# Kernel optimization log

Measured on AMD Instinct MI355X. Metric: run time of the kernel, lower is better.

Reference implementation:

```python
import jax, jax.numpy as jnp
import numpy as np

D_X = 16
D_L = 8
T_LEN = 131072
BIN_THRES = 0.1


def setup_inputs() -> dict:
    key = jax.random.key(0)
    ks = jax.random.split(key, 24)
    n = lambda k, shp, sc=0.1: jax.random.normal(k, shp, jnp.float32) * sc
    inp = {
        "latent_mean": jax.random.normal(ks[0], (2, T_LEN, D_L), jnp.float32),
        "latent_logvar": jax.random.normal(ks[1], (2, T_LEN, D_L), jnp.float32),
        "T": jax.random.uniform(ks[2], (T_LEN, 1), jnp.float32),
        # curr_adj_encoder: MLP(1 -> d_L -> d_L -> d_L*d_X), lrelu
        "cw0": n(ks[3], (1, D_L)), "cb0": n(ks[4], (D_L,)),
        "cw1": n(ks[5], (D_L, D_L)), "cb1": n(ks[6], (D_L,)),
        "cw2": n(ks[7], (D_L, D_L * D_X)), "cb2": n(ks[8], (D_L * D_X,)),
        # pre_adj_encoder
        "pw0": n(ks[9], (1, D_L)), "pb0": n(ks[10], (D_L,)),
        "pw1": n(ks[11], (D_L, D_L)), "pb1": n(ks[12], (D_L,)),
        "pw2": n(ks[13], (D_L, D_L * D_X)), "pb2": n(ks[14], (D_L * D_X,)),
        # latent_mean_out: FeatureExtractor(d_L,128,relu) + Linear(128,d_L)
        "fmw1": n(ks[15], (D_L, 128)), "fmb1": jnp.zeros((128,), jnp.float32),
        "fmw2": n(ks[16], (128, D_L)), "fmb2": jnp.zeros((D_L,), jnp.float32),
        # latent_logvar_out
        "fvw1": n(ks[17], (D_L, 128)), "fvb1": jnp.zeros((128,), jnp.float32),
        "fvw2": n(ks[18], (128, D_L)), "fvb2": jnp.zeros((D_L,), jnp.float32),
        # L2M per-node MLPs, batched over d_X: 4*d_L -> 64 -> 64 -> 1
        "lw0": n(ks[19], (D_X, 4 * D_L, 64)), "lb0": jnp.zeros((D_X, 64), jnp.float32),
        "lw1": n(ks[20], (D_X, 64, 64)), "lb1": jnp.zeros((D_X, 64), jnp.float32),
        "lw2": n(ks[21], (D_X, 64, 1)), "lb2": jnp.zeros((D_X, 1), jnp.float32),
    }
    return inp


def _forward(latent_mean, latent_logvar, T,
             cw0, cb0, cw1, cb1, cw2, cb2,
             pw0, pb0, pw1, pb1, pw2, pb2,
             fmw1, fmb1, fmw2, fmb2,
             fvw1, fvb1, fvw2, fvb2,
             lw0, lb0, lw1, lb1, lw2, lb2):
    lrelu = jax.nn.leaky_relu

    def mlp(x, w0, b0, w1, b1, w2, b2):
        h = lrelu(x @ w0 + b0)
        h = lrelu(h @ w1 + b1)
        return h @ w2 + b2

    Ct = mlp(T, cw0, cb0, cw1, cb1, cw2, cb2).reshape(-1, D_X, D_L)
    Ct_1 = mlp(T, pw0, pb0, pw1, pb1, pw2, pb2).reshape(-1, D_X, D_L)
    # Only Ct is binarized in the original forward (Ct_1 stays continuous).
    Ct = jnp.where(Ct < BIN_THRES, 0.0, 1.0).astype(Ct.dtype)

    zeros = jnp.zeros_like(latent_mean[:, :1, :])
    lm_prev = jnp.concatenate([zeros, latent_mean[:, :-1, :]], axis=1)
    lv_prev = jnp.concatenate([zeros, latent_logvar[:, :-1, :]], axis=1)

    def head(x, w1, b1, w2, b2):
        return jax.nn.relu(x @ w1 + b1) @ w2 + b2

    lm_pred = head(latent_mean, fmw1, fmb1, fmw2, fmb2)
    lv_pred = head(latent_logvar, fvw1, fvb1, fvw2, fvb2)

    def decode(lm, lv, C):
        # C: [T, d_X, d_L]; lm/lv: [2, T, d_L]
        def gather(x):
            g = jnp.einsum('ijk,lik->lijk', C, x)          # [2, T, d_X, d_L]
            g = jnp.transpose(g, (1, 2, 3, 0))              # [T, d_X, d_L, 2]
            return g.reshape(x.shape[1], D_X, 2 * D_L)
        h = jnp.concatenate([gather(lm), gather(lv)], axis=-1)  # [T, d_X, 4*d_L]
        h = jax.nn.relu(jnp.einsum('tnf,nfo->tno', h, lw0) + lb0)
        h = jnp.einsum('tnf,nfo->tno', h, lw1) + lb1             # last decoder layer: no relu
        h = jnp.einsum('tnf,nfo->tno', h, lw2) + lb2             # [T, d_X, 1]
        return jax.nn.relu(h[..., 0])                             # [T, d_X]

    recon = decode(latent_mean, latent_logvar, Ct)
    pred = decode(lm_prev, lv_prev, Ct_1)
    return recon, pred, lm_pred, lv_pred, Ct, Ct_1


def reference(latent_mean, latent_logvar, T,
              cw0, cb0, cw1, cb1, cw2, cb2,
              pw0, pb0, pw1, pb1, pw2, pb2,
              fmw1, fmb1, fmw2, fmb2,
              fvw1, fvb1, fvw2, fvb2,
              lw0, lb0, lw1, lb1, lw2, lb2):
    return _forward(latent_mean, latent_logvar, T,
                    cw0, cb0, cw1, cb1, cw2, cb2,
                    pw0, pb0, pw1, pb1, pw2, pb2,
                    fmw1, fmb1, fmw2, fmb2,
                    fvw1, fvb1, fvw2, fvb2,
                    lw0, lb0, lw1, lb1, lw2, lb2)
```

## Files before the change

### kernel.cpp

```cpp
#include <hip/hip_runtime.h>
#include <math.h>

#define TL 131072

static constexpr size_t OFF_RECON = 0;
static constexpr size_t OFF_PRED  = (size_t)TL * 16;
static constexpr size_t OFF_LMP   = (size_t)TL * 32;
static constexpr size_t OFF_LVP   = (size_t)TL * 48;
static constexpr size_t OFF_CT    = (size_t)TL * 64;
static constexpr size_t OFF_CT1   = (size_t)TL * 192;

typedef _Float16 h2 __attribute__((ext_vector_type(2)));
typedef _Float16 h8 __attribute__((ext_vector_type(8)));
typedef float f32x4 __attribute__((ext_vector_type(4)));

struct Params {
  const float* lm;  const float* lv;  const float* Tin;
  const float* cw0; const float* cb0; const float* cw1; const float* cb1; const float* cw2; const float* cb2;
  const float* pw0; const float* pb0; const float* pw1; const float* pb1; const float* pw2; const float* pb2;
  const float* fmw1; const float* fmb1; const float* fmw2; const float* fmb2;
  const float* fvw1; const float* fvb1; const float* fvw2; const float* fvb2;
  const float* lw0; const float* lb0; const float* lw1; const float* lb1; const float* lw2; const float* lb2;
  const float* w12src;
  float* out;
};

__device__ __forceinline__ const float4* rc4(const float* p) { return reinterpret_cast<const float4*>(p); }
__device__ __forceinline__ float4*       rw4(float* p)       { return reinterpret_cast<float4*>(p); }

__device__ __forceinline__ void load8(const float* __restrict__ src, float* dst) {
  float4 a = rc4(src)[0], b = rc4(src)[1];
  dst[0]=a.x; dst[1]=a.y; dst[2]=a.z; dst[3]=a.w;
  dst[4]=b.x; dst[5]=b.y; dst[6]=b.z; dst[7]=b.w;
}
__device__ __forceinline__ void store8(float* __restrict__ dst, const float* v) {
  rw4(dst)[0] = make_float4(v[0],v[1],v[2],v[3]);
  rw4(dst)[1] = make_float4(v[4],v[5],v[6],v[7]);
}
__device__ __forceinline__ void store16(float* __restrict__ dst, const float* v) {
  rw4(dst)[0] = make_float4(v[0],v[1],v[2],v[3]);
  rw4(dst)[1] = make_float4(v[4],v[5],v[6],v[7]);
  rw4(dst)[2] = make_float4(v[8],v[9],v[10],v[11]);
  rw4(dst)[3] = make_float4(v[12],v[13],v[14],v[15]);
}

union PU { h2 h; uint32_t u; };
union U4 { uint32_t u[4]; h2 h[4]; h8 v; uint4 q; };

__device__ __forceinline__ h2 pack2(float a, float b) {
  h2 r; r[0] = (_Float16)a; r[1] = (_Float16)b; return r;
}

__global__ __launch_bounds__(256) void tld_prep(const float* __restrict__ lw1,
                                                const float* __restrict__ lw2,
                                                const float* __restrict__ lb1,
                                                const float* __restrict__ lb2,
                                                float* __restrict__ ws) {
  const int tid = threadIdx.x;
  #pragma unroll 1
  for (int i = tid; i < 1024; i += 256) {
    int n = i >> 6, h = i & 63;
    float s = 0.f;
    #pragma unroll 8
    for (int o = 0; o < 64; ++o)
      s = fmaf(lw1[n * 4096 + h * 64 + o], lw2[n * 64 + o], s);
    ws[i] = s;
  }
  if (tid < 16) {
    float b = lb2[tid];
    #pragma unroll 8
    for (int o = 0; o < 64; ++o)
      b = fmaf(lb1[tid * 64 + o], lw2[tid * 64 + o], b);
    ws[1024 + tid] = b;
  }
}

__global__ __launch_bounds__(256, 2) void tld_fused(Params p) {
  __shared__ __align__(16) float     s_w12[1024];
  __shared__ __align__(16) float     s_b12[16];
  __shared__ __align__(16) float     s_lb0[1024];
  __shared__ __align__(16) float     s_ew2t[128 * 8];
  __shared__ __align__(16) float     s_eb2b[128];
  __shared__ __align__(16) float     s_hw1t[2][1024];
  __shared__ __align__(16) float     s_hw2[2][1024];
  __shared__ __align__(16) float     s_hb1[2][128];
  __shared__ __align__(16) float     s_hb2[2][8];
  __shared__ __align__(16) _Float16  s_W[2][64 * 40];
  __shared__ __align__(16) uint32_t  s_dl[129 * 20];
  __shared__ __align__(16) float     s_e1[128 * 12];
  __shared__ __align__(16) unsigned long long s_msk[128 * 3];
  __shared__ __align__(16) float     s_res[4][16 * 68];

  const int tid = threadIdx.x;
  const int B   = blockIdx.x * 128;

  rw4(s_lb0)[tid]    = rc4(p.lb0)[tid];
  rw4(s_hw2[0])[tid] = rc4(p.fmw2)[tid];
  rw4(s_hw2[1])[tid] = rc4(p.fvw2)[tid];
  if (tid < 32)       { rw4(s_hb1[0])[tid] = rc4(p.fmb1)[tid]; }
  else if (tid < 64)  { rw4(s_hb1[1])[tid - 32] = rc4(p.fvb1)[tid - 32]; }
  else if (tid < 96)  { rw4(s_eb2b)[tid - 64] = rc4(p.pb2)[tid - 64]; }
  else if (tid < 100) { int q = tid - 96; rw4(s_hb2[q >> 1])[q & 1] = rc4((q >> 1) ? p.fvb2 : p.fmb2)[q & 1]; }
  #pragma unroll 1
  for (int i = tid; i < 2048; i += 256) {
    int r = i >> 10, ii = i & 1023, o = ii >> 3, f = ii & 7;
    s_hw1t[r][ii] = (r ? p.fvw1 : p.fmw1)[f * 128 + o];
  }
  if (tid < 128) {
    #pragma unroll
    for (int i = 0; i < 8; ++i) s_ew2t[tid * 8 + i] = p.pw2[i * 128 + tid];
  }
  if (p.w12src) {
    rw4(s_w12)[tid] = rc4(p.w12src)[tid];
    if (tid < 4) rw4(s_b12)[tid] = rc4(p.w12src + 1024)[tid];
  } else {
    #pragma unroll 1
    for (int i = tid; i < 1024; i += 256) {
      int n = i >> 6, h = i & 63;
      float s = 0.f;
      for (int o = 0; o < 64; ++o)
        s = fmaf(p.lw1[n * 4096 + h * 64 + o], p.lw2[n * 64 + o], s);
      s_w12[i] = s;
    }
    if (tid < 16) {
      float b = p.lb2[tid];
      for (int o = 0; o < 64; ++o)
        b = fmaf(p.lb1[tid * 64 + o], p.lw2[tid * 64 + o], b);
      s_b12[tid] = b;
    }
  }
  const int wk  = tid & 31;
  const int wj0 = (tid >> 5) * 8;
  {
    const float4* g = rc4(p.lw0);
    float4 wa = g[wk * 16 + (tid >> 5) * 2];
    float4 wb = g[wk * 16 + (tid >> 5) * 2 + 1];
    _Float16* dW = s_W[0];
    dW[(wj0 + 0) * 40 + wk] = (_Float16)wa.x;
    dW[(wj0 + 1) * 40 + wk] = (_Float16)wa.y;
    dW[(wj0 + 2) * 40 + wk] = (_Float16)wa.z;
    dW[(wj0 + 3) * 40 + wk] = (_Float16)wa.w;
    dW[(wj0 + 4) * 40 + wk] = (_Float16)wb.x;
    dW[(wj0 + 5) * 40 + wk] = (_Float16)wb.y;
    dW[(wj0 + 6) * 40 + wk] = (_Float16)wb.z;
    dW[(wj0 + 7) * 40 + wk] = (_Float16)wb.w;
  }
  __syncthreads();

  const int u    = tid & 127;
  const int t    = B + u;
  const int role = __builtin_amdgcn_readfirstlane((int)(tid >> 7));
  const float Tt = p.Tin[t];

  unsigned long long cmlo = 0ull, cmhi = 0ull;
  float e1f[8];

  if (role == 0) {
    double e0d[8], e1d[8];
    const double Td = (double)Tt;
    #pragma unroll
    for (int j = 0; j < 8; ++j) {
      double v = Td * (double)p.cw0[j] + (double)p.cb0[j];
      e0d[j] = v < 0.0 ? 0.01 * v : v;
    }
    #pragma unroll
    for (int j = 0; j < 8; ++j) {
      double v = (double)p.cb1[j];
      #pragma unroll
      for (int i = 0; i < 8; ++i) v = fma(e0d[i], (double)p.cw1[i * 8 + j], v);
      e1d[j] = v < 0.0 ? 0.01 * v : v;
    }
    #pragma unroll 1
    for (int n2 = 0; n2 < 8; ++n2) {
      float cb[16];
      #pragma unroll
      for (int kk = 0; kk < 16; ++kk) {
        const int nk = n2 * 16 + kk;
        double s = (double)p.cb2[nk];
        #pragma unroll
        for (int i = 0; i < 8; ++i)
          s = fma(e1d[i], (double)p.cw2[i * 128 + nk], s);
        const int b = (s < 0.1) ? 0 : 1;
        cb[kk] = (float)b;
        if (nk < 64) cmlo |= (unsigned long long)b << nk;
        else         cmhi |= (unsigned long long)b << (nk - 64);
      }
      store16(p.out + OFF_CT + (size_t)t * 128 + n2 * 16, cb);
    }
    s_msk[u * 3]     = cmlo;
    s_msk[u * 3 + 1] = cmhi;
  } else {
    float e0[8];
    #pragma unroll
    for (int j = 0; j < 8; ++j) {
      float v = fmaf(Tt, p.pw0[j], p.pb0[j]);
      e0[j] = v < 0.f ? 0.01f * v : v;
    }
    #pragma unroll
    for (int j = 0; j < 8; ++j) {
      float v = p.pb1[j];
      #pragma unroll
      for (int i = 0; i < 8; ++i) v = fmaf(e0[i], p.pw1[i * 8 + j], v);
      e1f[j] = v < 0.f ? 0.01f * v : v;
    }
    {
      float4* d = (float4*)&s_e1[u * 12];
      d[0] = make_float4(e1f[0], e1f[1], e1f[2], e1f[3]);
      d[1] = make_float4(e1f[4], e1f[5], e1f[6], e1f[7]);
    }
    #pragma unroll 1
    for (int n2 = 0; n2 < 8; ++n2) {
      float cb[16];
      #pragma unroll
      for (int kk = 0; kk < 16; ++kk) {
        const int nk = n2 * 16 + kk;
        const float4* w = (const float4*)&s_ew2t[nk * 8];
        float4 x0 = w[0], x1 = w[1];
        float s = s_eb2b[nk];
        s = fmaf(e1f[0], x0.x, s); s = fmaf(e1f[1], x0.y, s);
        s = fmaf(e1f[2], x0.z, s); s = fmaf(e1f[3], x0.w, s);
        s = fmaf(e1f[4], x1.x, s); s = fmaf(e1f[5], x1.y, s);
        s = fmaf(e1f[6], x1.z, s); s = fmaf(e1f[7], x1.w, s);
        cb[kk] = s;
      }
      store16(p.out + OFF_CT1 + (size_t)t * 128 + n2 * 16, cb);
    }
  }

  float dl[4][8];
  if (role == 0) {
    load8(p.lm + (size_t)t * 8, dl[0]);
    load8(p.lm + (size_t)TL * 8 + (size_t)t * 8, dl[1]);
    load8(p.lv + (size_t)t * 8, dl[2]);
    load8(p.lv + (size_t)TL * 8 + (size_t)t * 8, dl[3]);
  } else {
    if (t > 0) {
      load8(p.lm + (size_t)(t - 1) * 8, dl[0]);
      load8(p.lm + (size_t)TL * 8 + (size_t)(t - 1) * 8, dl[1]);
      load8(p.lv + (size_t)(t - 1) * 8, dl[2]);
      load8(p.lv + (size_t)TL * 8 + (size_t)(t - 1) * 8, dl[3]);
    } else {
      #pragma unroll
      for (int r = 0; r < 4; ++r)
        #pragma unroll
        for (int j = 0; j < 8; ++j) dl[r][j] = 0.f;
    }
  }
  {
    const int slot = (role == 0) ? (u + 1) : (u == 0 ? 0 : -1);
    if (slot >= 0) {
      uint32_t dw[16];
      #pragma unroll
      for (int k = 0; k < 8; ++k) {
        PU a; a.h = pack2(dl[0][k], dl[1][k]); dw[k]     = a.u;
        PU b; b.h = pack2(dl[2][k], dl[3][k]); dw[8 + k] = b.u;
      }
      uint4* dst = (uint4*)&s_dl[slot * 20];
      dst[0] = make_uint4(dw[0], dw[1], dw[2], dw[3]);
      dst[1] = make_uint4(dw[4], dw[5], dw[6], dw[7]);
      dst[2] = make_uint4(dw[8], dw[9], dw[10], dw[11]);
      dst[3] = make_uint4(dw[12], dw[13], dw[14], dw[15]);
    }
  }

  {
    float hx[2][8];
    if (role == 0) {
      #pragma unroll
      for (int j = 0; j < 8; ++j) { hx[0][j] = dl[0][j]; hx[1][j] = dl[1][j]; }
    } else {
      load8(p.lv + (size_t)t * 8, hx[0]);
      load8(p.lv + (size_t)TL * 8 + (size_t)t * 8, hx[1]);
    }
    float acc8[2][8];
    #pragma unroll
    for (int l = 0; l < 2; ++l)
      #pragma unroll
      for (int j = 0; j < 8; ++j) acc8[l][j] = s_hb2[role][j];
    const float* w1t = s_hw1t[role];
    const float* w2r = s_hw2[role];
    const float* b1  = s_hb1[role];
    #pragma unroll 1
    for (int o = 0; o < 128; ++o) {
      float4 u0 = rc4(w1t)[o * 2], u1 = rc4(w1t)[o * 2 + 1];
      const float wf[8] = {u0.x,u0.y,u0.z,u0.w,u1.x,u1.y,u1.z,u1.w};
      const float bo = b1[o];
      float a0 = bo, a1 = bo;
      #pragma unroll
      for (int f = 0; f < 8; ++f) {
        a0 = fmaf(hx[0][f], wf[f], a0);
        a1 = fmaf(hx[1][f], wf[f], a1);
      }
      a0 = fmaxf(a0, 0.f); a1 = fmaxf(a1, 0.f);
      float4 v0 = rc4(w2r)[o * 2], v1 = rc4(w2r)[o * 2 + 1];
      const float w2f[8] = {v0.x,v0.y,v0.z,v0.w,v1.x,v1.y,v1.z,v1.w};
      #pragma unroll
      for (int j = 0; j < 8; ++j) {
        acc8[0][j] = fmaf(a0, w2f[j], acc8[0][j]);
        acc8[1][j] = fmaf(a1, w2f[j], acc8[1][j]);
      }
    }
    const size_t hbase = role ? OFF_LVP : OFF_LMP;
    store8(p.out + hbase + (size_t)t * 8, acc8[0]);
    store8(p.out + hbase + (size_t)TL * 8 + (size_t)t * 8, acc8[1]);
  }

  __syncthreads();

  const int w     = tid >> 6;
  const int lane  = tid & 63;
  const int drole = __builtin_amdgcn_readfirstlane(w >> 1);
  const int tl0   = (w & 1) * 64;
  const int l15   = lane & 15;
  const int g     = lane >> 4;
  const int kb    = (g & 1) * 4;
  float* res = s_res[w];

  #pragma unroll 1
  for (int n = 0; n < 16; ++n) {
    float4 wa, wb;
    if (n < 15) {
      const float4* gsrc = rc4(p.lw0 + (size_t)(n + 1) * 2048);
      wa = gsrc[wk * 16 + (tid >> 5) * 2];
      wb = gsrc[wk * 16 + (tid >> 5) * 2 + 1];
    }
    float cwv[4][8];
    if (drole == 1) {
      #pragma unroll
      for (int q = 0; q < 4; ++q) {
        const float4* ww = (const float4*)&s_ew2t[(n * 8 + kb + q) * 8];
        float4 x0 = ww[0], x1 = ww[1];
        cwv[q][0]=x0.x; cwv[q][1]=x0.y; cwv[q][2]=x0.z; cwv[q][3]=x0.w;
        cwv[q][4]=x1.x; cwv[q][5]=x1.y; cwv[q][6]=x1.z; cwv[q][7]=x1.w;
      }
    }
    const _Float16* Wcur = s_W[n & 1];
    h8 Bf[4];
    float bias[4], w12v[4];
    #pragma unroll
    for (int ji = 0; ji < 4; ++ji) {
      Bf[ji]   = *(const h8*)&Wcur[(ji * 16 + l15) * 40 + g * 8];
      bias[ji] = s_lb0[n * 64 + ji * 16 + l15];
      w12v[ji] = s_w12[n * 64 + ji * 16 + l15];
    }
    h8 Af[4];
    #pragma unroll
    for (int ti = 0; ti < 4; ++ti) {
      const int tloc = tl0 + ti * 16 + l15;
      const int slot = tloc + 1 - drole;
      U4 dv; dv.q = *(const uint4*)&s_dl[slot * 20 + g * 4];
      U4 xf;
      if (drole == 0) {
        const unsigned long long m = s_msk[tloc * 3 + (n >> 3)];
        const unsigned byte = (unsigned)(m >> ((n & 7) * 8)) & 0xffu;
        #pragma unroll
        for (int q = 0; q < 4; ++q)
          xf.u[q] = ((byte >> (kb + q)) & 1u) ? dv.u[q] : 0u;
      } else {
        const float4* e = (const float4*)&s_e1[tloc * 12];
        float4 e0 = e[0], e1v = e[1];
        const float ef[8] = {e0.x,e0.y,e0.z,e0.w,e1v.x,e1v.y,e1v.z,e1v.w};
        #pragma unroll
        for (int q = 0; q < 4; ++q) {
          float c = s_eb2b[n * 8 + kb + q];
          #pragma unroll
          for (int i = 0; i < 8; ++i) c = fmaf(ef[i], cwv[q][i], c);
          xf.h[q] = pack2(c, c) * dv.h[q];
        }
      }
      Af[ti] = xf.v;
    }
    const float b12n = s_b12[n];
    #pragma unroll
    for (int ti = 0; ti < 4; ++ti) {
      f32x4 d0, d1, d2, d3;
      d0[0]=bias[0]; d0[1]=bias[0]; d0[2]=bias[0]; d0[3]=bias[0];
      d1[0]=bias[1]; d1[1]=bias[1]; d1[2]=bias[1]; d1[3]=bias[1];
      d2[0]=bias[2]; d2[1]=bias[2]; d2[2]=bias[2]; d2[3]=bias[2];
      d3[0]=bias[3]; d3[1]=bias[3]; d3[2]=bias[3]; d3[3]=bias[3];
      d0 = __builtin_amdgcn_mfma_f32_16x16x32_f16(Af[ti], Bf[0], d0, 0, 0, 0);
      d1 = __builtin_amdgcn_mfma_f32_16x16x32_f16(Af[ti], Bf[1], d1, 0, 0, 0);
      d2 = __builtin_amdgcn_mfma_f32_16x16x32_f16(Af[ti], Bf[2], d2, 0, 0, 0);
      d3 = __builtin_amdgcn_mfma_f32_16x16x32_f16(Af[ti], Bf[3], d3, 0, 0, 0);
      float pr[4];
      #pragma unroll
      for (int reg = 0; reg < 4; ++reg) {
        float s = fmaxf(d0[reg], 0.f) * w12v[0];
        s = fmaf(fmaxf(d1[reg], 0.f), w12v[1], s);
        s = fmaf(fmaxf(d2[reg], 0.f), w12v[2], s);
        s = fmaf(fmaxf(d3[reg], 0.f), w12v[3], s);
        pr[reg] = s;
      }
      #pragma unroll
      for (int m = 1; m < 16; m <<= 1) {
        #pragma unroll
        for (int reg = 0; reg < 4; ++reg)
          pr[reg] += __shfl_xor(pr[reg], m, 64);
      }
      #pragma unroll
      for (int reg = 0; reg < 4; ++reg)
        pr[reg] = fmaxf(b12n + pr[reg], 0.f);
      if (l15 == 0) {
        float4* d = (float4*)&res[n * 68 + ti * 16 + g * 4];
        d[0] = make_float4(pr[0], pr[1], pr[2], pr[3]);
      }
    }
    if (n < 15) {
      _Float16* dW = s_W[(n + 1) & 1];
      dW[(wj0 + 0) * 40 + wk] = (_Float16)wa.x;
      dW[(wj0 + 1) * 40 + wk] = (_Float16)wa.y;
      dW[(wj0 + 2) * 40 + wk] = (_Float16)wa.z;
      dW[(wj0 + 3) * 40 + wk] = (_Float16)wa.w;
      dW[(wj0 + 4) * 40 + wk] = (_Float16)wb.x;
      dW[(wj0 + 5) * 40 + wk] = (_Float16)wb.y;
      dW[(wj0 + 6) * 40 + wk] = (_Float16)wb.z;
      dW[(wj0 + 7) * 40 + wk] = (_Float16)wb.w;
    }
    __syncthreads();
  }

  {
    float o16[16];
    #pragma unroll
    for (int n = 0; n < 16; ++n) o16[n] = res[n * 68 + lane];
    const size_t r_off = drole ? OFF_PRED : OFF_RECON;
    store16(p.out + r_off + (size_t)(B + tl0 + lane) * 16, o16);
  }
}

extern "C" void kernel_launch(void* const* d_in, const int* in_sizes, int n_in,
                              void* d_out, int out_size, void* d_ws, size_t ws_size,
                              hipStream_t stream) {
  Params p;
  p.lm   = (const float*)d_in[0];
  p.lv   = (const float*)d_in[1];
  p.Tin  = (const float*)d_in[2];
  p.cw0  = (const float*)d_in[3];  p.cb0 = (const float*)d_in[4];
  p.cw1  = (const float*)d_in[5];  p.cb1 = (const float*)d_in[6];
  p.cw2  = (const float*)d_in[7];  p.cb2 = (const float*)d_in[8];
  p.pw0  = (const float*)d_in[9];  p.pb0 = (const float*)d_in[10];
  p.pw1  = (const float*)d_in[11]; p.pb1 = (const float*)d_in[12];
  p.pw2  = (const float*)d_in[13]; p.pb2 = (const float*)d_in[14];
  p.fmw1 = (const float*)d_in[15]; p.fmb1 = (const float*)d_in[16];
  p.fmw2 = (const float*)d_in[17]; p.fmb2 = (const float*)d_in[18];
  p.fvw1 = (const float*)d_in[19]; p.fvb1 = (const float*)d_in[20];
  p.fvw2 = (const float*)d_in[21]; p.fvb2 = (const float*)d_in[22];
  p.lw0  = (const float*)d_in[23]; p.lb0 = (const float*)d_in[24];
  p.lw1  = (const float*)d_in[25]; p.lb1 = (const float*)d_in[26];
  p.lw2  = (const float*)d_in[27]; p.lb2 = (const float*)d_in[28];
  p.out  = (float*)d_out;

  const bool use_ws = ws_size >= 1040 * sizeof(float);
  if (use_ws) {
    tld_prep<<<dim3(1), dim3(256), 0, stream>>>(p.lw1, p.lw2, p.lb1, p.lb2, (float*)d_ws);
    p.w12src = (const float*)d_ws;
  } else {
    p.w12src = nullptr;
  }
  tld_fused<<<dim3(TL / 128), dim3(256), 0, stream>>>(p);
}
```

Measured before the change: 466.8 us.

## Swap MFMA operand roles, read C from global, alias LDS to raise occupancy

```diff
diff --git a/kernel.cpp b/kernel.cpp
--- a/kernel.cpp
+++ b/kernel.cpp
@@ -44,7 +44,6 @@
   rw4(dst)[3] = make_float4(v[12],v[13],v[14],v[15]);
 }
 
-union PU { h2 h; uint32_t u; };
 union U4 { uint32_t u[4]; h2 h[4]; h8 v; uint4 q; };
 
 __device__ __forceinline__ h2 pack2(float a, float b) {
@@ -75,36 +74,35 @@
   }
 }
 
-__global__ __launch_bounds__(256, 2) void tld_fused(Params p) {
-  __shared__ __align__(16) float     s_w12[1024];
-  __shared__ __align__(16) float     s_b12[16];
-  __shared__ __align__(16) float     s_lb0[1024];
-  __shared__ __align__(16) float     s_ew2t[128 * 8];
-  __shared__ __align__(16) float     s_eb2b[128];
-  __shared__ __align__(16) float     s_hw1t[2][1024];
-  __shared__ __align__(16) float     s_hw2[2][1024];
-  __shared__ __align__(16) float     s_hb1[2][128];
-  __shared__ __align__(16) float     s_hb2[2][8];
-  __shared__ __align__(16) _Float16  s_W[2][64 * 40];
-  __shared__ __align__(16) uint32_t  s_dl[129 * 20];
-  __shared__ __align__(16) float     s_e1[128 * 12];
-  __shared__ __align__(16) unsigned long long s_msk[128 * 3];
-  __shared__ __align__(16) float     s_res[4][16 * 68];
+__global__ __launch_bounds__(256, 4) void tld_fused(Params p) {
+  __shared__ __align__(16) _Float16 s_W[2][64 * 40];
+  __shared__ __align__(16) float    s_w12[1024];
+  __shared__ __align__(16) float    s_b12[16];
+  __shared__ __align__(16) float    s_lb0[1024];
+  __shared__ __align__(16) char     s_pool[22080];
+
+  float* s_hw1t = (float*)s_pool;
+  float* s_hw2  = (float*)(s_pool + 8192);
+  float* s_hb1  = (float*)(s_pool + 16384);
+  float* s_hb2  = (float*)(s_pool + 17408);
+  float* s_ew2t = (float*)(s_pool + 17472);
+  float* s_eb2b = (float*)(s_pool + 21568);
+  _Float16* s_resh = (_Float16*)s_pool;
 
   const int tid = threadIdx.x;
   const int B   = blockIdx.x * 128;
 
-  rw4(s_lb0)[tid]    = rc4(p.lb0)[tid];
-  rw4(s_hw2[0])[tid] = rc4(p.fmw2)[tid];
-  rw4(s_hw2[1])[tid] = rc4(p.fvw2)[tid];
-  if (tid < 32)       { rw4(s_hb1[0])[tid] = rc4(p.fmb1)[tid]; }
-  else if (tid < 64)  { rw4(s_hb1[1])[tid - 32] = rc4(p.fvb1)[tid - 32]; }
+  rw4(s_lb0)[tid]          = rc4(p.lb0)[tid];
+  rw4(s_hw2)[tid]          = rc4(p.fmw2)[tid];
+  rw4(s_hw2 + 1024)[tid]   = rc4(p.fvw2)[tid];
+  if (tid < 32)       { rw4(s_hb1)[tid] = rc4(p.fmb1)[tid]; }
+  else if (tid < 64)  { rw4(s_hb1 + 128)[tid - 32] = rc4(p.fvb1)[tid - 32]; }
   else if (tid < 96)  { rw4(s_eb2b)[tid - 64] = rc4(p.pb2)[tid - 64]; }
-  else if (tid < 100) { int q = tid - 96; rw4(s_hb2[q >> 1])[q & 1] = rc4((q >> 1) ? p.fvb2 : p.fmb2)[q & 1]; }
+  else if (tid < 100) { int q = tid - 96; rw4(s_hb2 + (q >> 1) * 8)[q & 1] = rc4((q >> 1) ? p.fvb2 : p.fmb2)[q & 1]; }
   #pragma unroll 1
   for (int i = tid; i < 2048; i += 256) {
     int r = i >> 10, ii = i & 1023, o = ii >> 3, f = ii & 7;
-    s_hw1t[r][ii] = (r ? p.fvw1 : p.fmw1)[f * 128 + o];
+    s_hw1t[r * 1024 + ii] = (r ? p.fvw1 : p.fmw1)[f * 128 + o];
   }
   if (tid < 128) {
     #pragma unroll
@@ -152,9 +150,6 @@
   const int role = __builtin_amdgcn_readfirstlane((int)(tid >> 7));
   const float Tt = p.Tin[t];
 
-  unsigned long long cmlo = 0ull, cmhi = 0ull;
-  float e1f[8];
-
   if (role == 0) {
     double e0d[8], e1d[8];
     const double Td = (double)Tt;
@@ -180,17 +175,12 @@
         #pragma unroll
         for (int i = 0; i < 8; ++i)
           s = fma(e1d[i], (double)p.cw2[i * 128 + nk], s);
-        const int b = (s < 0.1) ? 0 : 1;
-        cb[kk] = (float)b;
-        if (nk < 64) cmlo |= (unsigned long long)b << nk;
-        else         cmhi |= (unsigned long long)b << (nk - 64);
+        cb[kk] = (s < 0.1) ? 0.f : 1.f;
       }
       store16(p.out + OFF_CT + (size_t)t * 128 + n2 * 16, cb);
     }
-    s_msk[u * 3]     = cmlo;
-    s_msk[u * 3 + 1] = cmhi;
   } else {
-    float e0[8];
+    float e0[8], e1f[8];
     #pragma unroll
     for (int j = 0; j < 8; ++j) {
       float v = fmaf(Tt, p.pw0[j], p.pb0[j]);
@@ -202,11 +192,6 @@
       #pragma unroll
       for (int i = 0; i < 8; ++i) v = fmaf(e0[i], p.pw1[i * 8 + j], v);
       e1f[j] = v < 0.f ? 0.01f * v : v;
-    }
-    {
-      float4* d = (float4*)&s_e1[u * 12];
-      d[0] = make_float4(e1f[0], e1f[1], e1f[2], e1f[3]);
-      d[1] = make_float4(e1f[4], e1f[5], e1f[6], e1f[7]);
     }
     #pragma unroll 1
     for (int n2 = 0; n2 < 8; ++n2) {
@@ -227,59 +212,24 @@
     }
   }
 
-  float dl[4][8];
-  if (role == 0) {
-    load8(p.lm + (size_t)t * 8, dl[0]);
-    load8(p.lm + (size_t)TL * 8 + (size_t)t * 8, dl[1]);
-    load8(p.lv + (size_t)t * 8, dl[2]);
-    load8(p.lv + (size_t)TL * 8 + (size_t)t * 8, dl[3]);
-  } else {
-    if (t > 0) {
-      load8(p.lm + (size_t)(t - 1) * 8, dl[0]);
-      load8(p.lm + (size_t)TL * 8 + (size_t)(t - 1) * 8, dl[1]);
-      load8(p.lv + (size_t)(t - 1) * 8, dl[2]);
-      load8(p.lv + (size_t)TL * 8 + (size_t)(t - 1) * 8, dl[3]);
-    } else {
-      #pragma unroll
-      for (int r = 0; r < 4; ++r)
-        #pragma unroll
-        for (int j = 0; j < 8; ++j) dl[r][j] = 0.f;
-    }
-  }
-  {
-    const int slot = (role == 0) ? (u + 1) : (u == 0 ? 0 : -1);
-    if (slot >= 0) {
-      uint32_t dw[16];
-      #pragma unroll
-      for (int k = 0; k < 8; ++k) {
-        PU a; a.h = pack2(dl[0][k], dl[1][k]); dw[k]     = a.u;
-        PU b; b.h = pack2(dl[2][k], dl[3][k]); dw[8 + k] = b.u;
-      }
-      uint4* dst = (uint4*)&s_dl[slot * 20];
-      dst[0] = make_uint4(dw[0], dw[1], dw[2], dw[3]);
-      dst[1] = make_uint4(dw[4], dw[5], dw[6], dw[7]);
-      dst[2] = make_uint4(dw[8], dw[9], dw[10], dw[11]);
-      dst[3] = make_uint4(dw[12], dw[13], dw[14], dw[15]);
-    }
-  }
-
   {
     float hx[2][8];
     if (role == 0) {
-      #pragma unroll
-      for (int j = 0; j < 8; ++j) { hx[0][j] = dl[0][j]; hx[1][j] = dl[1][j]; }
+      load8(p.lm + (size_t)t * 8, hx[0]);
+      load8(p.lm + (size_t)TL * 8 + (size_t)t * 8, hx[1]);
     } else {
       load8(p.lv + (size_t)t * 8, hx[0]);
       load8(p.lv + (size_t)TL * 8 + (size_t)t * 8, hx[1]);
     }
+    const float* w1t  = s_hw1t + role * 1024;
+    const float* w2r  = s_hw2  + role * 1024;
+    const float* b1   = s_hb1  + role * 128;
+    const float* hb2r = s_hb2  + role * 8;
     float acc8[2][8];
     #pragma unroll
     for (int l = 0; l < 2; ++l)
       #pragma unroll
-      for (int j = 0; j < 8; ++j) acc8[l][j] = s_hb2[role][j];
-    const float* w1t = s_hw1t[role];
-    const float* w2r = s_hw2[role];
-    const float* b1  = s_hb1[role];
+      for (int j = 0; j < 8; ++j) acc8[l][j] = hb2r[j];
     #pragma unroll 1
     for (int o = 0; o < 128; ++o) {
       float4 u0 = rc4(w1t)[o * 2], u1 = rc4(w1t)[o * 2 + 1];
@@ -314,7 +264,27 @@
   const int l15   = lane & 15;
   const int g     = lane >> 4;
   const int kb    = (g & 1) * 4;
-  float* res = s_res[w];
+  const float* xbase = (g < 2) ? p.lm : p.lv;
+  const float* Cbuf  = p.out + (drole ? OFF_CT1 : OFF_CT);
+  _Float16* resw = s_resh + w * 1088;
+
+  int trow[4];
+  U4 dv[4];
+  #pragma unroll
+  for (int ti = 0; ti < 4; ++ti) {
+    trow[ti] = B + tl0 + ti * 16 + l15;
+    const int src = trow[ti] - drole;
+    const int s0  = src < 0 ? 0 : src;
+    float4 v0 = rc4(xbase + (size_t)s0 * 8 + kb)[0];
+    float4 v1 = rc4(xbase + (size_t)TL * 8 + (size_t)s0 * 8 + kb)[0];
+    U4 dd;
+    dd.h[0] = pack2(v0.x, v1.x);
+    dd.h[1] = pack2(v0.y, v1.y);
+    dd.h[2] = pack2(v0.z, v1.z);
+    dd.h[3] = pack2(v0.w, v1.w);
+    if (src < 0) dd.q = make_uint4(0u, 0u, 0u, 0u);
+    dv[ti] = dd;
+  }
 
   #pragma unroll 1
   for (int n = 0; n < 16; ++n) {
@@ -324,87 +294,70 @@
       wa = gsrc[wk * 16 + (tid >> 5) * 2];
       wb = gsrc[wk * 16 + (tid >> 5) * 2 + 1];
     }
-    float cwv[4][8];
-    if (drole == 1) {
-      #pragma unroll
-      for (int q = 0; q < 4; ++q) {
-        const float4* ww = (const float4*)&s_ew2t[(n * 8 + kb + q) * 8];
-        float4 x0 = ww[0], x1 = ww[1];
-        cwv[q][0]=x0.x; cwv[q][1]=x0.y; cwv[q][2]=x0.z; cwv[q][3]=x0.w;
-        cwv[q][4]=x1.x; cwv[q][5]=x1.y; cwv[q][6]=x1.z; cwv[q][7]=x1.w;
-      }
-    }
     const _Float16* Wcur = s_W[n & 1];
-    h8 Bf[4];
-    float bias[4], w12v[4];
-    #pragma unroll
-    for (int ji = 0; ji < 4; ++ji) {
-      Bf[ji]   = *(const h8*)&Wcur[(ji * 16 + l15) * 40 + g * 8];
-      bias[ji] = s_lb0[n * 64 + ji * 16 + l15];
-      w12v[ji] = s_w12[n * 64 + ji * 16 + l15];
-    }
-    h8 Af[4];
+    h8 Af0 = *(const h8*)&Wcur[( 0 + l15) * 40 + g * 8];
+    h8 Af1 = *(const h8*)&Wcur[(16 + l15) * 40 + g * 8];
+    h8 Af2 = *(const h8*)&Wcur[(32 + l15) * 40 + g * 8];
+    h8 Af3 = *(const h8*)&Wcur[(48 + l15) * 40 + g * 8];
+    const float b12n = s_b12[n];
+
     #pragma unroll
     for (int ti = 0; ti < 4; ++ti) {
-      const int tloc = tl0 + ti * 16 + l15;
-      const int slot = tloc + 1 - drole;
-      U4 dv; dv.q = *(const uint4*)&s_dl[slot * 20 + g * 4];
-      U4 xf;
-      if (drole == 0) {
-        const unsigned long long m = s_msk[tloc * 3 + (n >> 3)];
-        const unsigned byte = (unsigned)(m >> ((n & 7) * 8)) & 0xffu;
-        #pragma unroll
-        for (int q = 0; q < 4; ++q)
-          xf.u[q] = ((byte >> (kb + q)) & 1u) ? dv.u[q] : 0u;
-      } else {
-        const float4* e = (const float4*)&s_e1[tloc * 12];
-        float4 e0 = e[0], e1v = e[1];
-        const float ef[8] = {e0.x,e0.y,e0.z,e0.w,e1v.x,e1v.y,e1v.z,e1v.w};
-        #pragma unroll
-        for (int q = 0; q < 4; ++q) {
-          float c = s_eb2b[n * 8 + kb + q];
-          #pragma unroll
-          for (int i = 0; i < 8; ++i) c = fmaf(ef[i], cwv[q][i], c);
-          xf.h[q] = pack2(c, c) * dv.h[q];
-        }
-      }
-      Af[ti] = xf.v;
-    }
-    const float b12n = s_b12[n];
-    #pragma unroll
-    for (int ti = 0; ti < 4; ++ti) {
-      f32x4 d0, d1, d2, d3;
-      d0[0]=bias[0]; d0[1]=bias[0]; d0[2]=bias[0]; d0[3]=bias[0];
-      d1[0]=bias[1]; d1[1]=bias[1]; d1[2]=bias[1]; d1[3]=bias[1];
-      d2[0]=bias[2]; d2[1]=bias[2]; d2[2]=bias[2]; d2[3]=bias[2];
-      d3[0]=bias[3]; d3[1]=bias[3]; d3[2]=bias[3]; d3[3]=bias[3];
-      d0 = __builtin_amdgcn_mfma_f32_16x16x32_f16(Af[ti], Bf[0], d0, 0, 0, 0);
-      d1 = __builtin_amdgcn_mfma_f32_16x16x32_f16(Af[ti], Bf[1], d1, 0, 0, 0);
-      d2 = __builtin_amdgcn_mfma_f32_16x16x32_f16(Af[ti], Bf[2], d2, 0, 0, 0);
-      d3 = __builtin_amdgcn_mfma_f32_16x16x32_f16(Af[ti], Bf[3], d3, 0, 0, 0);
-      float pr[4];
-      #pragma unroll
-      for (int reg = 0; reg < 4; ++reg) {
-        float s = fmaxf(d0[reg], 0.f) * w12v[0];
-        s = fmaf(fmaxf(d1[reg], 0.f), w12v[1], s);
-        s = fmaf(fmaxf(d2[reg], 0.f), w12v[2], s);
-        s = fmaf(fmaxf(d3[reg], 0.f), w12v[3], s);
-        pr[reg] = s;
-      }
-      #pragma unroll
-      for (int m = 1; m < 16; m <<= 1) {
-        #pragma unroll
-        for (int reg = 0; reg < 4; ++reg)
-          pr[reg] += __shfl_xor(pr[reg], m, 64);
-      }
-      #pragma unroll
-      for (int reg = 0; reg < 4; ++reg)
-        pr[reg] = fmaxf(b12n + pr[reg], 0.f);
-      if (l15 == 0) {
-        float4* d = (float4*)&res[n * 68 + ti * 16 + g * 4];
-        d[0] = make_float4(pr[0], pr[1], pr[2], pr[3]);
-      }
-    }
+      float4 cc = rc4(Cbuf + (size_t)trow[ti] * 128 + n * 8 + kb)[0];
+      U4 bx;
+      bx.h[0] = pack2(cc.x, cc.x) * dv[ti].h[0];
+      bx.h[1] = pack2(cc.y, cc.y) * dv[ti].h[1];
+      bx.h[2] = pack2(cc.z, cc.z) * dv[ti].h[2];
+      bx.h[3] = pack2(cc.w, cc.w) * dv[ti].h[3];
+      const h8 Bf = bx.v;
+
+      float partial = 0.f;
+      {
+        float4 bias = rc4(s_lb0 + n * 64 +  0 + g * 4)[0];
+        f32x4 d; d[0]=bias.x; d[1]=bias.y; d[2]=bias.z; d[3]=bias.w;
+        d = __builtin_amdgcn_mfma_f32_16x16x32_f16(Af0, Bf, d, 0, 0, 0);
+        float4 wv = rc4(s_w12 + n * 64 +  0 + g * 4)[0];
+        partial = fmaf(fmaxf(d[0],0.f), wv.x, partial);
+        partial = fmaf(fmaxf(d[1],0.f), wv.y, partial);
+        partial = fmaf(fmaxf(d[2],0.f), wv.z, partial);
+        partial = fmaf(fmaxf(d[3],0.f), wv.w, partial);
+      }
+      {
+        float4 bias = rc4(s_lb0 + n * 64 + 16 + g * 4)[0];
+        f32x4 d; d[0]=bias.x; d[1]=bias.y; d[2]=bias.z; d[3]=bias.w;
+        d = __builtin_amdgcn_mfma_f32_16x16x32_f16(Af1, Bf, d, 0, 0, 0);
+        float4 wv = rc4(s_w12 + n * 64 + 16 + g * 4)[0];
+        partial = fmaf(fmaxf(d[0],0.f), wv.x, partial);
+        partial = fmaf(fmaxf(d[1],0.f), wv.y, partial);
+        partial = fmaf(fmaxf(d[2],0.f), wv.z, partial);
+        partial = fmaf(fmaxf(d[3],0.f), wv.w, partial);
+      }
+      {
+        float4 bias = rc4(s_lb0 + n * 64 + 32 + g * 4)[0];
+        f32x4 d; d[0]=bias.x; d[1]=bias.y; d[2]=bias.z; d[3]=bias.w;
+        d = __builtin_amdgcn_mfma_f32_16x16x32_f16(Af2, Bf, d, 0, 0, 0);
+        float4 wv = rc4(s_w12 + n * 64 + 32 + g * 4)[0];
+        partial = fmaf(fmaxf(d[0],0.f), wv.x, partial);
+        partial = fmaf(fmaxf(d[1],0.f), wv.y, partial);
+        partial = fmaf(fmaxf(d[2],0.f), wv.z, partial);
+        partial = fmaf(fmaxf(d[3],0.f), wv.w, partial);
+      }
+      {
+        float4 bias = rc4(s_lb0 + n * 64 + 48 + g * 4)[0];
+        f32x4 d; d[0]=bias.x; d[1]=bias.y; d[2]=bias.z; d[3]=bias.w;
+        d = __builtin_amdgcn_mfma_f32_16x16x32_f16(Af3, Bf, d, 0, 0, 0);
+        float4 wv = rc4(s_w12 + n * 64 + 48 + g * 4)[0];
+        partial = fmaf(fmaxf(d[0],0.f), wv.x, partial);
+        partial = fmaf(fmaxf(d[1],0.f), wv.y, partial);
+        partial = fmaf(fmaxf(d[2],0.f), wv.z, partial);
+        partial = fmaf(fmaxf(d[3],0.f), wv.w, partial);
+      }
+      partial += __shfl_xor(partial, 16, 64);
+      partial += __shfl_xor(partial, 32, 64);
+      const float r = fmaxf(b12n + partial, 0.f);
+      if (lane < 16) resw[n * 68 + ti * 16 + l15] = (_Float16)r;
+    }
+
     if (n < 15) {
       _Float16* dW = s_W[(n + 1) & 1];
       dW[(wj0 + 0) * 40 + wk] = (_Float16)wa.x;
@@ -422,7 +375,7 @@
   {
     float o16[16];
     #pragma unroll
-    for (int n = 0; n < 16; ++n) o16[n] = res[n * 68 + lane];
+    for (int n = 0; n < 16; ++n) o16[n] = (float)resw[n * 68 + lane];
     const size_t r_off = drole ? OFF_PRED : OFF_RECON;
     store16(p.out + r_off + (size_t)(B + tl0 + lane) * 16, o16);
   }
```

Result: no change. 469.4 us (+0.6%).
